# Kernel tuning notes

Hardware: AMD Instinct MI355X
Metric: run time of the kernel (lower is better)

Reference implementation:

```python
import jax, jax.numpy as jnp
import numpy as np

TEMP = 0.07  # softmax temperature T


def _l2norm(x, axis=1, eps=1e-12):
    return x / jnp.clip(jnp.linalg.norm(x, axis=axis, keepdims=True), eps, None)


def setup_inputs() -> dict:
    key = jax.random.key(0)
    k1, k2, k3, k4 = jax.random.split(key, 4)
    B, K, D = 256, 8192, 128
    q = jax.random.normal(k1, (B, D), dtype=jnp.float32)
    ba_queue = _l2norm(jax.random.normal(k2, (K, D), dtype=jnp.float32))
    nonba_queue = _l2norm(jax.random.normal(k3, (K, D), dtype=jnp.float32))
    targets = jax.random.randint(k4, (B,), 0, 2, dtype=jnp.int64)
    return {"q": q, "ba_queue": ba_queue, "nonba_queue": nonba_queue, "targets": targets}


def reference(q, ba_queue, nonba_queue, targets):
    K = ba_queue.shape[0]
    # encoder output is L2-normalized; queues are detached buffers
    qn = _l2norm(q, axis=1)
    all_feature = jnp.concatenate([qn, ba_queue, nonba_queue], axis=0)  # [N, D]
    all_label = jnp.concatenate([
        targets.astype(jnp.int32),
        jnp.ones((K,), dtype=jnp.int32),
        jnp.zeros((K,), dtype=jnp.int32),
    ])  # [N]
    N = all_feature.shape[0]

    # [N, N] similarity logits
    sim = jnp.matmul(all_feature, all_feature.T) / TEMP
    logits = sim - jax.lax.stop_gradient(jnp.max(sim, axis=1, keepdims=True))

    # positive mask (same label), excluding self
    mask = (all_label[:, None] == all_label[None, :]).astype(jnp.float32)
    logits_mask = 1.0 - jnp.eye(N, dtype=jnp.float32)
    mask = mask * logits_mask

    exp_logits = jnp.exp(logits) * logits_mask
    log_prob = logits - jnp.log(jnp.sum(exp_logits, axis=1, keepdims=True))
    mean_log_prob_pos = jnp.sum(mask * log_prob, axis=1) / jnp.sum(mask, axis=1)
    return -jnp.mean(mean_log_prob_pos)
```

## Files before the change

kernel.cpp:

```cpp
#include <hip/hip_runtime.h>
#include <hip/hip_bf16.h>
#include <stdint.h>

#define TEMPERATURE 0.07f
#define SC 20.6099312f

constexpr int NQ = 256;
constexpr int KQ = 8192;
constexpr int D  = 128;
constexpr int N  = NQ + 2 * KQ;
constexpr int CS = 26;
constexpr int BN = 128;
constexpr int NT = N / BN;
constexpr int RBM = N / 128;
constexpr int RBF = N / 256;

typedef float f32x16 __attribute__((ext_vector_type(16)));
typedef int   i32x4  __attribute__((ext_vector_type(4)));
typedef int   i32x8  __attribute__((ext_vector_type(8)));

constexpr size_t OFF_F32  = 0;
constexpr size_t OFF_8    = OFF_F32  + (size_t)N * D * 4;
constexpr size_t OFF_8S   = OFF_8    + (size_t)N * D;
constexpr size_t OFF_PART = OFF_8S   + (size_t)N * D;
constexpr size_t OFF_LP   = OFF_PART + (size_t)CS * N * 4;
constexpr size_t OFF_BSUM = OFF_LP   + (size_t)260 * 2 * 128 * 4;

__global__ __launch_bounds__(256) void k_prep(const float* __restrict__ q,
                                              const float* __restrict__ ba,
                                              const float* __restrict__ nb,
                                              const long long* __restrict__ tgt,
                                              float* __restrict__ ff,
                                              unsigned char* __restrict__ fb8,
                                              unsigned char* __restrict__ fb8s,
                                              float* __restrict__ lp) {
    __shared__ float red[4][2][128];
    int wid = threadIdx.x >> 6, lane = threadIdx.x & 63;
    int rbase = blockIdx.x * 64 + wid * 16;
    float s0x = 0.f, s0y = 0.f, s1x = 0.f, s1y = 0.f;
    for (int i = 0; i < 16; ++i) {
        int r = rbase + i;
        const float* src = (r < NQ) ? (q + (size_t)r * D)
                         : (r < NQ + KQ) ? (ba + (size_t)(r - NQ) * D)
                         : (nb + (size_t)(r - NQ - KQ) * D);
        float2 v = *(const float2*)(src + lane * 2);
        float a = v.x, b = v.y;
        int lab;
        if (r < NQ) {
            float ss = a * a + b * b;
            #pragma unroll
            for (int m = 1; m < 64; m <<= 1) ss += __shfl_xor(ss, m);
            float scale = 1.0f / fmaxf(sqrtf(ss), 1e-12f);
            a *= scale; b *= scale;
            lab = (int)tgt[r];
        } else {
            lab = (r < NQ + KQ) ? 1 : 0;
        }
        *(float2*)(ff + (size_t)r * D + lane * 2) = make_float2(a, b);
        int w8  = __builtin_amdgcn_cvt_pk_fp8_f32(a, b, 0, false);
        int w8s = __builtin_amdgcn_cvt_pk_fp8_f32(a * SC, b * SC, 0, false);
        *(unsigned short*)(fb8  + (size_t)r * D + lane * 2) = (unsigned short)w8;
        *(unsigned short*)(fb8s + (size_t)r * D + lane * 2) = (unsigned short)w8s;
        if (lab) { s1x += a; s1y += b; } else { s0x += a; s0y += b; }
    }
    red[wid][0][lane * 2]     = s0x;
    red[wid][0][lane * 2 + 1] = s0y;
    red[wid][1][lane * 2]     = s1x;
    red[wid][1][lane * 2 + 1] = s1y;
    __syncthreads();
    int lab2 = threadIdx.x >> 7, d = threadIdx.x & 127;
    float s = red[0][lab2][d] + red[1][lab2][d] + red[2][lab2][d] + red[3][lab2][d];
    lp[((size_t)blockIdx.x * 2 + lab2) * 128 + d] = s;
}

__global__ __launch_bounds__(256, 3) void k_main(const unsigned char* __restrict__ fb8,
                                                 const unsigned char* __restrict__ fb8s,
                                                 float* __restrict__ part) {
    __shared__ __align__(16) unsigned char lds[2][BN * 128];
    const int bid = blockIdx.x;
    const int rb = bid / CS, cs = bid % CS;
    const int tid = threadIdx.x;
    const int lane = tid & 63;
    const int wid  = tid >> 6;
    const int wr = wid >> 1, wc = wid & 1;
    const int l31 = lane & 31, lhi = lane >> 5;
    const int rw = rb * 128 + wr * 64;

    int soff[4];
    #pragma unroll
    for (int i = 0; i < 4; ++i) {
        int flat = i * 256 + tid;
        int line = flat >> 4, p = flat & 15;
        int pl = p ^ (line & 15);
        soff[i] = (2 * line + (pl >> 3)) * 128 + (pl & 7) * 16;
    }

    i32x8 rf[2][2];
    #pragma unroll
    for (int rs = 0; rs < 2; ++rs)
        #pragma unroll
        for (int s = 0; s < 2; ++s)
            rf[rs][s] = *(const i32x8*)(fb8s + (size_t)(rw + rs * 32 + l31) * D + s * 64 + lhi * 32);

    float rsum[2] = {0.f, 0.f};

    {
        const unsigned char* base = fb8 + (size_t)cs * (BN * 128);
        #pragma unroll
        for (int i = 0; i < 4; ++i)
            __builtin_amdgcn_global_load_lds(
                (const __attribute__((address_space(1))) unsigned int*)(base + soff[i]),
                (__attribute__((address_space(3))) unsigned int*)(&lds[0][(i * 256 + tid) * 16]),
                16, 0, 0);
    }
    asm volatile("s_waitcnt vmcnt(0)" ::: "memory");
    __builtin_amdgcn_s_barrier();

    int cur = 0;
    for (int t = 0; t < 5; ++t) {
        int ct = cs + t * CS;

        if (t + 1 < 5) {
            const unsigned char* base = fb8 + ((size_t)ct + CS) * (BN * 128);
            #pragma unroll
            for (int i = 0; i < 4; ++i)
                __builtin_amdgcn_global_load_lds(
                    (const __attribute__((address_space(1))) unsigned int*)(base + soff[i]),
                    (__attribute__((address_space(3))) unsigned int*)(&lds[cur ^ 1][(i * 256 + tid) * 16]),
                    16, 0, 0);
        }

        f32x16 acc[2][2];
        #pragma unroll
        for (int i = 0; i < 2; ++i)
            #pragma unroll
            for (int j = 0; j < 2; ++j)
                #pragma unroll
                for (int e = 0; e < 16; ++e) acc[i][j][e] = -SC;

        __builtin_amdgcn_s_setprio(1);
        #pragma unroll
        for (int s = 0; s < 2; ++s) {
            #pragma unroll
            for (int cc = 0; cc < 2; ++cc) {
                int crow = wc * 64 + cc * 32 + l31;
                int line = crow >> 1;
                int pb = ((crow & 1) << 3) + s * 4 + lhi * 2;
                const unsigned char* lb = &lds[cur][line * 256];
                i32x4 lo = *(const i32x4*)(lb + ((pb    ) ^ (line & 15)) * 16);
                i32x4 hi = *(const i32x4*)(lb + ((pb + 1) ^ (line & 15)) * 16);
                i32x8 a = {lo[0], lo[1], lo[2], lo[3], hi[0], hi[1], hi[2], hi[3]};
                acc[cc][0] = __builtin_amdgcn_mfma_scale_f32_32x32x64_f8f6f4(
                    a, rf[0][s], acc[cc][0], 0, 0, 0, 0x7f7f7f7f, 0, 0x7f7f7f7f);
                acc[cc][1] = __builtin_amdgcn_mfma_scale_f32_32x32x64_f8f6f4(
                    a, rf[1][s], acc[cc][1], 0, 0, 0, 0x7f7f7f7f, 0, 0x7f7f7f7f);
            }
        }
        __builtin_amdgcn_s_setprio(0);

        #pragma unroll
        for (int cc = 0; cc < 2; ++cc) {
            #pragma unroll
            for (int rs = 0; rs < 2; ++rs) {
                float p = 0.f;
                #pragma unroll
                for (int g = 0; g < 16; ++g)
                    p += __builtin_amdgcn_exp2f(acc[cc][rs][g]);
                rsum[rs] += p;
            }
        }

        asm volatile("s_waitcnt vmcnt(0)" ::: "memory");
        __builtin_amdgcn_s_barrier();
        cur ^= 1;
    }

    rsum[0] += __shfl_xor(rsum[0], 32);
    rsum[1] += __shfl_xor(rsum[1], 32);
    __shared__ float xred[2][2][32];
    if (wc == 0 && lane < 32) {
        xred[wr][0][lane] = rsum[0];
        xred[wr][1][lane] = rsum[1];
    }
    __syncthreads();
    if (wc == 1 && lane < 32) {
        part[(size_t)cs * N + rw + lane]      = xred[wr][0][lane] + rsum[0];
        part[(size_t)cs * N + rw + 32 + lane] = xred[wr][1][lane] + rsum[1];
    }
}

__global__ __launch_bounds__(256) void k_rowfin(const float* __restrict__ part,
                                                const float* __restrict__ ff,
                                                const float* __restrict__ lp,
                                                const long long* __restrict__ tgt,
                                                float* __restrict__ bsum) {
    __shared__ float sS[256];
    __shared__ float red[256];
    __shared__ int scnt[2];
    {
        int lab = threadIdx.x >> 7, d = threadIdx.x & 127;
        float s[4] = {0.f, 0.f, 0.f, 0.f};
        for (int b = 0; b < 260; b += 4) {
            #pragma unroll
            for (int j = 0; j < 4; ++j)
                s[j] += lp[((size_t)(b + j) * 2 + lab) * 128 + d];
        }
        sS[threadIdx.x] = (s[0] + s[1]) + (s[2] + s[3]);
        if (threadIdx.x < 64) {
            int c = 0;
            #pragma unroll
            for (int i = 0; i < 4; ++i) c += (int)tgt[threadIdx.x + 64 * i];
            #pragma unroll
            for (int m = 1; m < 64; m <<= 1) c += __shfl_xor(c, m);
            if (threadIdx.x == 0) { scnt[0] = (NQ - c) + KQ; scnt[1] = c + KQ; }
        }
    }
    __syncthreads();
    int r = blockIdx.x * 256 + threadIdx.x;
    float se = 0.f;
    #pragma unroll
    for (int c = 0; c < CS; ++c) se += part[(size_t)c * N + r];
    int lab = (r < NQ) ? (int)tgt[r] : ((r < NQ + KQ) ? 1 : 0);
    const float4* frow = (const float4*)(ff + (size_t)r * D);
    const float4* srow = (const float4*)(sS + lab * 128);
    float dS = 0.f, dd = 0.f;
    #pragma unroll
    for (int i = 0; i < 32; ++i) {
        float4 f = frow[i];
        float4 s = srow[i];
        dS += f.x * s.x + f.y * s.y + f.z * s.z + f.w * s.w;
        int wa  = __builtin_amdgcn_cvt_pk_fp8_f32(f.x, f.y, 0, false);
        int wb  = __builtin_amdgcn_cvt_pk_fp8_f32(f.z, f.w, 0, false);
        int wsa = __builtin_amdgcn_cvt_pk_fp8_f32(f.x * SC, f.y * SC, 0, false);
        int wsb = __builtin_amdgcn_cvt_pk_fp8_f32(f.z * SC, f.w * SC, 0, false);
        dd += __builtin_amdgcn_cvt_f32_fp8(wa, 0) * __builtin_amdgcn_cvt_f32_fp8(wsa, 0)
            + __builtin_amdgcn_cvt_f32_fp8(wa, 1) * __builtin_amdgcn_cvt_f32_fp8(wsa, 1)
            + __builtin_amdgcn_cvt_f32_fp8(wb, 0) * __builtin_amdgcn_cvt_f32_fp8(wsb, 0)
            + __builtin_amdgcn_cvt_f32_fp8(wb, 1) * __builtin_amdgcn_cvt_f32_fp8(wsb, 1);
    }
    se -= __builtin_amdgcn_exp2f(dd - SC);
    float lse = logf(se) + 1.0f / TEMPERATURE;
    float P = (float)(scnt[lab] - 1);
    float mlpp = (dS - 1.0f) / (TEMPERATURE * P) - lse;
    red[threadIdx.x] = mlpp;
    __syncthreads();
    for (int s2 = 128; s2 > 0; s2 >>= 1) {
        if (threadIdx.x < s2) red[threadIdx.x] += red[threadIdx.x + s2];
        __syncthreads();
    }
    if (threadIdx.x == 0) bsum[blockIdx.x] = red[0];
}

__global__ __launch_bounds__(64) void k_final(const float* __restrict__ bsum,
                                              float* __restrict__ out) {
    float s = bsum[threadIdx.x];
    if (threadIdx.x == 0) s += bsum[64];
    #pragma unroll
    for (int m = 1; m < 64; m <<= 1) s += __shfl_xor(s, m);
    if (threadIdx.x == 0) out[0] = -s / (float)N;
}

extern "C" void kernel_launch(void* const* d_in, const int* in_sizes, int n_in,
                              void* d_out, int out_size, void* d_ws, size_t ws_size,
                              hipStream_t stream) {
    const float* q       = (const float*)d_in[0];
    const float* ba      = (const float*)d_in[1];
    const float* nb      = (const float*)d_in[2];
    const long long* tgt = (const long long*)d_in[3];
    char* ws = (char*)d_ws;
    float*         ff   = (float*)(ws + OFF_F32);
    unsigned char* fb8  = (unsigned char*)(ws + OFF_8);
    unsigned char* fb8s = (unsigned char*)(ws + OFF_8S);
    float*         part = (float*)(ws + OFF_PART);
    float*         lp   = (float*)(ws + OFF_LP);
    float*         bsum = (float*)(ws + OFF_BSUM);

    k_prep  <<<260,      256, 0, stream>>>(q, ba, nb, tgt, ff, fb8, fb8s, lp);
    k_main  <<<RBM * CS, 256, 0, stream>>>(fb8, fb8s, part);
    k_rowfin<<<RBF,      256, 0, stream>>>(part, ff, lp, tgt, bsum);
    k_final <<<1,         64, 0, stream>>>(bsum, (float*)d_out);
}
```

Baseline: 77.95 us.

## Software-pipeline exp2 reduction with next tile MFMAs and skip fp32 queue copy

Unrolls the five-tile loop in k_main and double-buffers the accumulators so the exp2 reductions of one tile interleave with the MFMAs of the next, hiding transcendental latency behind matrix work. Accumulators now start at zero rather than a max offset; the lse and self-term correction are adjusted accordingly. k_prep stops writing normalized fp32 copies of the queue rows, and k_rowfin reads the queues straight from the inputs, cutting global write traffic. The extra accumulator set raises register pressure, so the occupancy hint is lowered from 3 to 2 blocks.

```diff
diff --git a/kernel.cpp b/kernel.cpp
--- a/kernel.cpp
+++ b/kernel.cpp
@@ -11,7 +11,6 @@
 constexpr int N  = NQ + 2 * KQ;
 constexpr int CS = 26;
 constexpr int BN = 128;
-constexpr int NT = N / BN;
 constexpr int RBM = N / 128;
 constexpr int RBF = N / 256;
 
@@ -20,11 +19,14 @@
 typedef int   i32x8  __attribute__((ext_vector_type(8)));
 
 constexpr size_t OFF_F32  = 0;
-constexpr size_t OFF_8    = OFF_F32  + (size_t)N * D * 4;
+constexpr size_t OFF_8    = OFF_F32  + (size_t)NQ * D * 4;
 constexpr size_t OFF_8S   = OFF_8    + (size_t)N * D;
 constexpr size_t OFF_PART = OFF_8S   + (size_t)N * D;
 constexpr size_t OFF_LP   = OFF_PART + (size_t)CS * N * 4;
 constexpr size_t OFF_BSUM = OFF_LP   + (size_t)260 * 2 * 128 * 4;
+
+#define MFMA8(a, b, c) __builtin_amdgcn_mfma_scale_f32_32x32x64_f8f6f4( \
+    (a), (b), (c), 0, 0, 0, 0x7f7f7f7f, 0, 0x7f7f7f7f)
 
 __global__ __launch_bounds__(256) void k_prep(const float* __restrict__ q,
                                               const float* __restrict__ ba,
@@ -53,10 +55,10 @@
             float scale = 1.0f / fmaxf(sqrtf(ss), 1e-12f);
             a *= scale; b *= scale;
             lab = (int)tgt[r];
+            *(float2*)(ff + (size_t)r * D + lane * 2) = make_float2(a, b);
         } else {
             lab = (r < NQ + KQ) ? 1 : 0;
         }
-        *(float2*)(ff + (size_t)r * D + lane * 2) = make_float2(a, b);
         int w8  = __builtin_amdgcn_cvt_pk_fp8_f32(a, b, 0, false);
         int w8s = __builtin_amdgcn_cvt_pk_fp8_f32(a * SC, b * SC, 0, false);
         *(unsigned short*)(fb8  + (size_t)r * D + lane * 2) = (unsigned short)w8;
@@ -73,7 +75,59 @@
     lp[((size_t)blockIdx.x * 2 + lab2) * 128 + d] = s;
 }
 
-__global__ __launch_bounds__(256, 3) void k_main(const unsigned char* __restrict__ fb8,
+__device__ __forceinline__ i32x8 lda(const unsigned char* buf, int wc, int l31,
+                                     int lhi, int s, int cc) {
+    int crow = wc * 64 + cc * 32 + l31;
+    int line = crow >> 1;
+    int pb = ((crow & 1) << 3) + s * 4 + lhi * 2;
+    const unsigned char* lb = buf + line * 256;
+    i32x4 lo = *(const i32x4*)(lb + ((pb    ) ^ (line & 15)) * 16);
+    i32x4 hi = *(const i32x4*)(lb + ((pb + 1) ^ (line & 15)) * 16);
+    i32x8 a = {lo[0], lo[1], lo[2], lo[3], hi[0], hi[1], hi[2], hi[3]};
+    return a;
+}
+
+#define FIN(c) if (dofin) { const f32x16& A = pacc[((c) >> 2) & 1][((c) >> 1) & 1]; \
+    float s_ = 0.f; \
+    _Pragma("unroll") \
+    for (int e = 0; e < 8; ++e) s_ += __builtin_amdgcn_exp2f(A[(((c) & 1) << 3) + e]); \
+    ps[((c) >> 1) & 1] += s_; }
+
+__device__ __forceinline__ void phase(const unsigned char* buf,
+                                      f32x16 (&acc)[2][2], const f32x16 (&pacc)[2][2],
+                                      const i32x8 (&rf)[2][2], const f32x16& z16,
+                                      int wc, int l31, int lhi, bool dofin,
+                                      float (&rsum)[2]) {
+    i32x8 a00 = lda(buf, wc, l31, lhi, 0, 0);
+    i32x8 a10 = lda(buf, wc, l31, lhi, 1, 0);
+    i32x8 a01 = lda(buf, wc, l31, lhi, 0, 1);
+    i32x8 a11 = lda(buf, wc, l31, lhi, 1, 1);
+    float ps[2] = {0.f, 0.f};
+    acc[0][0] = MFMA8(a00, rf[0][0], z16);       FIN(0)
+    acc[0][0] = MFMA8(a10, rf[0][1], acc[0][0]); FIN(1)
+    acc[0][1] = MFMA8(a00, rf[1][0], z16);       FIN(2)
+    acc[0][1] = MFMA8(a10, rf[1][1], acc[0][1]); FIN(3)
+    acc[1][0] = MFMA8(a01, rf[0][0], z16);       FIN(4)
+    acc[1][0] = MFMA8(a11, rf[0][1], acc[1][0]); FIN(5)
+    acc[1][1] = MFMA8(a01, rf[1][0], z16);       FIN(6)
+    acc[1][1] = MFMA8(a11, rf[1][1], acc[1][1]); FIN(7)
+    if (dofin) { rsum[0] += ps[0]; rsum[1] += ps[1]; }
+}
+
+__device__ __forceinline__ void fin_all(const f32x16 (&pacc)[2][2], float (&rsum)[2]) {
+    #pragma unroll
+    for (int cc = 0; cc < 2; ++cc)
+        #pragma unroll
+        for (int rs = 0; rs < 2; ++rs) {
+            float p = 0.f;
+            #pragma unroll
+            for (int g = 0; g < 16; ++g)
+                p += __builtin_amdgcn_exp2f(pacc[cc][rs][g]);
+            rsum[rs] += p;
+        }
+}
+
+__global__ __launch_bounds__(256, 2) void k_main(const unsigned char* __restrict__ fb8,
                                                  const unsigned char* __restrict__ fb8s,
                                                  float* __restrict__ part) {
     __shared__ __align__(16) unsigned char lds[2][BN * 128];
@@ -95,6 +149,17 @@
         soff[i] = (2 * line + (pl >> 3)) * 128 + (pl & 7) * 16;
     }
 
+#define STAGE(T, B) { \
+    const unsigned char* base_ = fb8 + ((size_t)(cs + (T) * CS)) * (BN * 128); \
+    _Pragma("unroll") \
+    for (int i_ = 0; i_ < 4; ++i_) \
+        __builtin_amdgcn_global_load_lds( \
+            (const __attribute__((address_space(1))) unsigned int*)(base_ + soff[i_]), \
+            (__attribute__((address_space(3))) unsigned int*)(&lds[B][(i_ * 256 + tid) * 16]), \
+            16, 0, 0); }
+
+#define SYNC() { asm volatile("s_waitcnt vmcnt(0)" ::: "memory"); __builtin_amdgcn_s_barrier(); }
+
     i32x8 rf[2][2];
     #pragma unroll
     for (int rs = 0; rs < 2; ++rs)
@@ -102,78 +167,28 @@
         for (int s = 0; s < 2; ++s)
             rf[rs][s] = *(const i32x8*)(fb8s + (size_t)(rw + rs * 32 + l31) * D + s * 64 + lhi * 32);
 
+    f32x16 z16;
+    #pragma unroll
+    for (int e = 0; e < 16; ++e) z16[e] = 0.f;
+
     float rsum[2] = {0.f, 0.f};
-
-    {
-        const unsigned char* base = fb8 + (size_t)cs * (BN * 128);
-        #pragma unroll
-        for (int i = 0; i < 4; ++i)
-            __builtin_amdgcn_global_load_lds(
-                (const __attribute__((address_space(1))) unsigned int*)(base + soff[i]),
-                (__attribute__((address_space(3))) unsigned int*)(&lds[0][(i * 256 + tid) * 16]),
-                16, 0, 0);
-    }
-    asm volatile("s_waitcnt vmcnt(0)" ::: "memory");
-    __builtin_amdgcn_s_barrier();
-
-    int cur = 0;
-    for (int t = 0; t < 5; ++t) {
-        int ct = cs + t * CS;
-
-        if (t + 1 < 5) {
-            const unsigned char* base = fb8 + ((size_t)ct + CS) * (BN * 128);
-            #pragma unroll
-            for (int i = 0; i < 4; ++i)
-                __builtin_amdgcn_global_load_lds(
-                    (const __attribute__((address_space(1))) unsigned int*)(base + soff[i]),
-                    (__attribute__((address_space(3))) unsigned int*)(&lds[cur ^ 1][(i * 256 + tid) * 16]),
-                    16, 0, 0);
-        }
-
-        f32x16 acc[2][2];
-        #pragma unroll
-        for (int i = 0; i < 2; ++i)
-            #pragma unroll
-            for (int j = 0; j < 2; ++j)
-                #pragma unroll
-                for (int e = 0; e < 16; ++e) acc[i][j][e] = -SC;
-
-        __builtin_amdgcn_s_setprio(1);
-        #pragma unroll
-        for (int s = 0; s < 2; ++s) {
-            #pragma unroll
-            for (int cc = 0; cc < 2; ++cc) {
-                int crow = wc * 64 + cc * 32 + l31;
-                int line = crow >> 1;
-                int pb = ((crow & 1) << 3) + s * 4 + lhi * 2;
-                const unsigned char* lb = &lds[cur][line * 256];
-                i32x4 lo = *(const i32x4*)(lb + ((pb    ) ^ (line & 15)) * 16);
-                i32x4 hi = *(const i32x4*)(lb + ((pb + 1) ^ (line & 15)) * 16);
-                i32x8 a = {lo[0], lo[1], lo[2], lo[3], hi[0], hi[1], hi[2], hi[3]};
-                acc[cc][0] = __builtin_amdgcn_mfma_scale_f32_32x32x64_f8f6f4(
-                    a, rf[0][s], acc[cc][0], 0, 0, 0, 0x7f7f7f7f, 0, 0x7f7f7f7f);
-                acc[cc][1] = __builtin_amdgcn_mfma_scale_f32_32x32x64_f8f6f4(
-                    a, rf[1][s], acc[cc][1], 0, 0, 0, 0x7f7f7f7f, 0, 0x7f7f7f7f);
-            }
-        }
-        __builtin_amdgcn_s_setprio(0);
-
-        #pragma unroll
-        for (int cc = 0; cc < 2; ++cc) {
-            #pragma unroll
-            for (int rs = 0; rs < 2; ++rs) {
-                float p = 0.f;
-                #pragma unroll
-                for (int g = 0; g < 16; ++g)
-                    p += __builtin_amdgcn_exp2f(acc[cc][rs][g]);
-                rsum[rs] += p;
-            }
-        }
-
-        asm volatile("s_waitcnt vmcnt(0)" ::: "memory");
-        __builtin_amdgcn_s_barrier();
-        cur ^= 1;
-    }
+    f32x16 accA[2][2], accB[2][2];
+
+    STAGE(0, 0) SYNC()
+    STAGE(1, 1)
+    phase(lds[0], accA, accB, rf, z16, wc, l31, lhi, false, rsum);
+    SYNC()
+    STAGE(2, 0)
+    phase(lds[1], accB, accA, rf, z16, wc, l31, lhi, true, rsum);
+    SYNC()
+    STAGE(3, 1)
+    phase(lds[0], accA, accB, rf, z16, wc, l31, lhi, true, rsum);
+    SYNC()
+    STAGE(4, 0)
+    phase(lds[1], accB, accA, rf, z16, wc, l31, lhi, true, rsum);
+    SYNC()
+    phase(lds[0], accA, accB, rf, z16, wc, l31, lhi, true, rsum);
+    fin_all(accA, rsum);
 
     rsum[0] += __shfl_xor(rsum[0], 32);
     rsum[1] += __shfl_xor(rsum[1], 32);
@@ -187,10 +202,14 @@
         part[(size_t)cs * N + rw + lane]      = xred[wr][0][lane] + rsum[0];
         part[(size_t)cs * N + rw + 32 + lane] = xred[wr][1][lane] + rsum[1];
     }
+#undef STAGE
+#undef SYNC
 }
 
 __global__ __launch_bounds__(256) void k_rowfin(const float* __restrict__ part,
                                                 const float* __restrict__ ff,
+                                                const float* __restrict__ ba,
+                                                const float* __restrict__ nb,
                                                 const float* __restrict__ lp,
                                                 const long long* __restrict__ tgt,
                                                 float* __restrict__ bsum) {
@@ -221,7 +240,10 @@
     #pragma unroll
     for (int c = 0; c < CS; ++c) se += part[(size_t)c * N + r];
     int lab = (r < NQ) ? (int)tgt[r] : ((r < NQ + KQ) ? 1 : 0);
-    const float4* frow = (const float4*)(ff + (size_t)r * D);
+    const float* fsrc = (r < NQ) ? (ff + (size_t)r * D)
+                      : (r < NQ + KQ) ? (ba + (size_t)(r - NQ) * D)
+                      : (nb + (size_t)(r - NQ - KQ) * D);
+    const float4* frow = (const float4*)fsrc;
     const float4* srow = (const float4*)(sS + lab * 128);
     float dS = 0.f, dd = 0.f;
     #pragma unroll
@@ -238,8 +260,8 @@
             + __builtin_amdgcn_cvt_f32_fp8(wb, 0) * __builtin_amdgcn_cvt_f32_fp8(wsb, 0)
             + __builtin_amdgcn_cvt_f32_fp8(wb, 1) * __builtin_amdgcn_cvt_f32_fp8(wsb, 1);
     }
-    se -= __builtin_amdgcn_exp2f(dd - SC);
-    float lse = logf(se) + 1.0f / TEMPERATURE;
+    se -= __builtin_amdgcn_exp2f(dd);
+    float lse = logf(se);
     float P = (float)(scnt[lab] - 1);
     float mlpp = (dS - 1.0f) / (TEMPERATURE * P) - lse;
     red[threadIdx.x] = mlpp;
@@ -277,6 +299,6 @@
 
     k_prep  <<<260,      256, 0, stream>>>(q, ba, nb, tgt, ff, fb8, fb8s, lp);
     k_main  <<<RBM * CS, 256, 0, stream>>>(fb8, fb8s, part);
-    k_rowfin<<<RBF,      256, 0, stream>>>(part, ff, lp, tgt, bsum);
+    k_rowfin<<<RBF,      256, 0, stream>>>(part, ff, ba, nb, lp, tgt, bsum);
     k_final <<<1,         64, 0, stream>>>(bsum, (float*)d_out);
 }
```

Measured after the change: 79.68 us. 2.2% more time.
